# Kernel tuning notes

Hardware: AMD Instinct MI355X
Metric: run time of the kernel (lower is better)

Reference implementation:

```python
import jax, jax.numpy as jnp
import numpy as np

INPUT_DIM = 21
HIDDEN = 512
OUT_DIM = 20


def _lstm_cell(xt, h, c, Wx, bx, Wh):
    # xt: (B, in), h/c: (B, H); Wx: (4H, in), Wh: (4H, H), bx: (4H,)
    gates = xt @ Wx.T + bx + h @ Wh.T          # (B, 4H)
    i, f, g, o = jnp.split(gates, 4, axis=-1)   # torch chunk order: i, f, g, o
    i = jax.nn.sigmoid(i)
    f = jax.nn.sigmoid(f)
    g = jnp.tanh(g)
    o = jax.nn.sigmoid(o)
    c_new = f * c + i * g
    h_new = o * jnp.tanh(c_new)
    return h_new, c_new


def setup_inputs() -> dict:
    key = jax.random.key(0)
    ks = jax.random.split(key, 8)
    s_in = 1.0 / np.sqrt(INPUT_DIM)
    s_h = 1.0 / np.sqrt(HIDDEN)
    x = jax.random.normal(ks[0], (64, 1024, INPUT_DIM), dtype=jnp.float32)
    Wx0 = jax.random.uniform(ks[1], (4 * HIDDEN, INPUT_DIM), jnp.float32, -s_in, s_in)
    bx0 = jax.random.uniform(ks[2], (4 * HIDDEN,), jnp.float32, -s_in, s_in)
    Wh0 = jax.random.uniform(ks[3], (4 * HIDDEN, HIDDEN), jnp.float32, -s_h, s_h)
    Wx1 = jax.random.uniform(ks[4], (4 * HIDDEN, HIDDEN), jnp.float32, -s_h, s_h)
    bx1 = jax.random.uniform(ks[5], (4 * HIDDEN,), jnp.float32, -s_h, s_h)
    Wh1 = jax.random.uniform(ks[6], (4 * HIDDEN, HIDDEN), jnp.float32, -s_h, s_h)
    Wo = jax.random.uniform(ks[7], (OUT_DIM, HIDDEN), jnp.float32, -s_h, s_h)
    bo = jnp.zeros((OUT_DIM,), jnp.float32)
    return {"x": x, "Wx0": Wx0, "bx0": bx0, "Wh0": Wh0,
            "Wx1": Wx1, "bx1": bx1, "Wh1": Wh1, "Wo": Wo, "bo": bo}


def reference(x, Wx0, bx0, Wh0, Wx1, bx1, Wh1, Wo, bo):
    B, T, _ = x.shape
    H = Wh0.shape[1]
    h0 = jnp.zeros((B, H), x.dtype)
    c0 = jnp.zeros((B, H), x.dtype)
    h1 = jnp.zeros((B, H), x.dtype)
    c1 = jnp.zeros((B, H), x.dtype)

    def step(carry, xt):
        h0, c0, h1, c1 = carry
        h0, c0 = _lstm_cell(xt, h0, c0, Wx0, bx0, Wh0)
        h1, c1 = _lstm_cell(h0, h1, c1, Wx1, bx1, Wh1)
        out = jax.nn.sigmoid(h1 @ Wo.T + bo)  # (B, OUT_DIM)
        return (h0, c0, h1, c1), out

    _, outs = jax.lax.scan(step, (h0, c0, h1, c1), jnp.swapaxes(x, 0, 1))
    return jnp.swapaxes(outs, 0, 1)  # (B, T, OUT_DIM)
```

## Files before the change

kernel.cpp:

```cpp
#include <hip/hip_runtime.h>


#define T_STEPS 1024
#define WS_FLAG_OFF 0
#define WS_H0_OFF  4096
#define WS_H1_OFF  (4096 + 8*4*8192)
#define WS_NEED    (WS_H1_OFF + 8*2*8192)

#define SCOPE __HIP_MEMORY_SCOPE_AGENT

typedef _Float16 f16;
typedef _Float16 f16x8 __attribute__((ext_vector_type(8)));
typedef float    f32x4 __attribute__((ext_vector_type(4)));
typedef unsigned long long u64;

#define HP_STRIDE 520

__device__ __forceinline__ float sigm_(float x) {
    x = fminf(fmaxf(x, -30.f), 30.f);
    return 1.f / (1.f + __expf(-x));
}
__device__ __forceinline__ float tanh_(float x) {
    x = fminf(fmaxf(x, -15.f), 15.f);
    float e = __expf(-2.f * x);
    return (1.f - e) / (1.f + e);
}

__device__ __forceinline__ f16x8 afrag_lds(const f16* __restrict__ hp, int kbase,
                                           int b, int q) {
    return *(const f16x8*)(hp + (b & 7) * HP_STRIDE + kbase + q * 8);
}

__device__ __forceinline__ f16x8 pack8(const float* p) {
    float4 a = *(const float4*)p, b = *(const float4*)(p + 4);
    f16x8 f;
    f[0] = (f16)a.x; f[1] = (f16)a.y; f[2] = (f16)a.z; f[3] = (f16)a.w;
    f[4] = (f16)b.x; f[5] = (f16)b.y; f[6] = (f16)b.z; f[7] = (f16)b.w;
    return f;
}

__device__ __forceinline__ long long wait_flags(const int* f0, int t0,
                                                const int* f1, int t1, int lane,
                                                long long predict_clk) {
    const int* p = (lane & 16) ? (f1 + (lane & 15) * 4) : (f0 + (lane & 15) * 4);
    const int tgt = (lane & 16) ? t1 : t0;
    const bool act = (lane < 32);
    int v = act ? __hip_atomic_load(p, __ATOMIC_RELAXED, SCOPE)
                : 0x7fffffff;
    if (__all(v >= tgt)) return 0;
    long long t0c = (long long)__builtin_amdgcn_s_memtime();
    int rep = (int)(predict_clk >> 12);
    if (rep > 8) rep = 8;
    for (int i = 0; i < rep; ++i) __builtin_amdgcn_s_sleep(31);
    int spins = 0;
    for (;;) {
        v = act ? __hip_atomic_load(p, __ATOMIC_RELAXED, SCOPE)
                : 0x7fffffff;
        if (__all(v >= tgt)) break;
        ++spins;
        if (spins < 32)       __builtin_amdgcn_s_sleep(1);
        else if (spins < 256) __builtin_amdgcn_s_sleep(4);
        else                  __builtin_amdgcn_s_sleep(16);
        if (spins > (1 << 20)) break;
    }
    return (long long)__builtin_amdgcn_s_memtime() - t0c;
}

__device__ __forceinline__ long long ewma_upd(long long ew, long long d) {
    return ew - (ew >> 2) + (d >> 2);
}

__device__ __forceinline__ void stage_plane(const f16* __restrict__ gp,
                                            f16* __restrict__ dst, int tid) {
    const u64* g8 = (const u64*)gp;
    u64 v[4];
#pragma unroll
    for (int jj = 0; jj < 4; ++jj)
        v[jj] = __hip_atomic_load(g8 + jj * 256 + tid, __ATOMIC_RELAXED, SCOPE);
#pragma unroll
    for (int jj = 0; jj < 4; ++jj) {
        int i = jj * 256 + tid;
        int wg = i >> 6, b = (i >> 3) & 7, j = i & 7;
        *(u64*)(dst + b * HP_STRIDE + wg * 32 + j * 4) = v[jj];
    }
}

__device__ __forceinline__ void stage_two(const f16* __restrict__ gpA,
                                          f16* __restrict__ dstA,
                                          const f16* __restrict__ gpB,
                                          f16* __restrict__ dstB, int tid) {
    const u64* ga = (const u64*)gpA;
    const u64* gb = (const u64*)gpB;
    u64 va[4], vb[4];
#pragma unroll
    for (int jj = 0; jj < 4; ++jj)
        va[jj] = __hip_atomic_load(ga + jj * 256 + tid, __ATOMIC_RELAXED, SCOPE);
#pragma unroll
    for (int jj = 0; jj < 4; ++jj)
        vb[jj] = __hip_atomic_load(gb + jj * 256 + tid, __ATOMIC_RELAXED, SCOPE);
#pragma unroll
    for (int jj = 0; jj < 4; ++jj) {
        int i = jj * 256 + tid;
        int wg = i >> 6, b = (i >> 3) & 7, j = i & 7;
        *(u64*)(dstA + b * HP_STRIDE + wg * 32 + j * 4) = va[jj];
        *(u64*)(dstB + b * HP_STRIDE + wg * 32 + j * 4) = vb[jj];
    }
}

__device__ __forceinline__ f16x8 load_xfrag(const float* __restrict__ x,
                                            int gb8, int t, int ln, int q) {
    f16x8 f = {(_Float16)0, (_Float16)0, (_Float16)0, (_Float16)0,
               (_Float16)0, (_Float16)0, (_Float16)0, (_Float16)0};
    if (ln < 8 && t < T_STEPS) {
        const float* xp = x + ((size_t)(gb8 + ln) * 1024 + t) * 21;
#pragma unroll
        for (int j = 0; j < 8; ++j) {
            int kl = q * 8 + j;
            if (kl < 21) f[j] = (f16)xp[kl];
        }
    }
    return f;
}

__global__ void zero_ws_kernel(unsigned* __restrict__ p, int ndw) {
    int i = blockIdx.x * blockDim.x + threadIdx.x;
    int stride = gridDim.x * blockDim.x;
    for (; i < ndw; i += stride)
        __hip_atomic_store(p + i, 0u, __ATOMIC_RELAXED, SCOPE);
}

__global__ __launch_bounds__(256, 1)
void lstm_persist(const float* __restrict__ x,
                  const float* __restrict__ Wx0, const float* __restrict__ bx0,
                  const float* __restrict__ Wh0,
                  const float* __restrict__ Wx1, const float* __restrict__ bx1,
                  const float* __restrict__ Wh1,
                  const float* __restrict__ Wo,  const float* __restrict__ bo,
                  float* __restrict__ out, char* __restrict__ ws) {
    struct SM {
        float g[4][8][33];
        float c[8][32];
        float bias[4][32];
        __align__(8)  f16 hout[8][32];
        __align__(16) f16 planeA[8 * HP_STRIDE];
        __align__(16) f16 planeB[8 * HP_STRIDE];
        char  pad[60 * 1024];
    };
    __shared__ SM sm;
    const int tid = threadIdx.x;
    if (tid == 0x00FFFFFFu) sm.pad[0] = 1;

    const int bid  = blockIdx.x;
    const int g    = bid & 7;
    const int rk   = bid >> 3;
    const int role = rk >> 4;
    const int r    = rk & 15;
    const int w    = tid >> 6;
    const int lane = tid & 63;
    const int ln   = lane & 15;
    const int q    = lane >> 4;
    const int gb8  = g * 8;

    int* barb  = (int*)(ws + WS_FLAG_OFF) + g * 128;
    int* flag0 = barb;
    int* flag1 = barb + 64;
    f16* H0g = (f16*)(ws + WS_H0_OFF) + g * 16384;
    f16* H1g = (f16*)(ws + WS_H1_OFF) + g * 8192;

    ((float*)sm.c)[tid] = 0.f;
    if (tid < 128) {
        int gate = tid >> 5, u = tid & 31;
        const float* bx = role ? bx1 : bx0;
        sm.bias[gate][u] = bx[(gate << 9) + (r << 5) + u];
    }

    f16x8 W[64];
    if (role == 0) {
#pragma unroll
        for (int tau = 0; tau < 2; ++tau) {
            const int rw = (w << 9) + (r << 5) + tau * 16 + ln;
            const float* wh0r = Wh0 + (size_t)rw * 512;
#pragma unroll
            for (int kk = 0; kk < 16; ++kk)
                W[tau * 17 + kk] = pack8(wh0r + kk * 32 + q * 8);
            const float* wx0r = Wx0 + (size_t)rw * 21;
            f16x8 f = {(_Float16)0, (_Float16)0, (_Float16)0, (_Float16)0,
                       (_Float16)0, (_Float16)0, (_Float16)0, (_Float16)0};
#pragma unroll
            for (int j = 0; j < 8; ++j) {
                int kl = q * 8 + j;
                if (kl < 21) f[j] = (f16)wx0r[kl];
            }
            W[tau * 17 + 16] = f;
        }
    } else {
#pragma unroll
        for (int tau = 0; tau < 2; ++tau) {
            const int rw = (w << 9) + (r << 5) + tau * 16 + ln;
            const float* wx1r = Wx1 + (size_t)rw * 512;
            const float* wh1r = Wh1 + (size_t)rw * 512;
#pragma unroll
            for (int kk = 0; kk < 16; ++kk)
                W[tau * 32 + kk] = pack8(wx1r + kk * 32 + q * 8);
#pragma unroll
            for (int kk = 16; kk < 32; ++kk)
                W[tau * 32 + kk] = pack8(wh1r + (kk - 16) * 32 + q * 8);
        }
    }
    __syncthreads();

    if (role == 0) {
        long long ew = 0;
        for (int t = 0; t < T_STEPS; ++t) {
            const int wr = t & 3, rd = (t + 3) & 3;
            f16x8 xf = load_xfrag(x, gb8, t, ln, q);
            if (tid < 64) {
                long long d = wait_flags(flag0, t, flag1, t - 3, lane, ew);
                ew = ewma_upd(ew, d);
            }
            __syncthreads();
            stage_plane(H0g + rd * 4096, sm.planeA, tid);
            __syncthreads();

            f32x4 a0 = {0, 0, 0, 0}, a1 = {0, 0, 0, 0};
#pragma unroll
            for (int kk = 0; kk < 16; ++kk) {
                f16x8 A = afrag_lds(sm.planeA, kk * 32, ln, q);
                a0 = __builtin_amdgcn_mfma_f32_16x16x32_f16(A, W[kk], a0, 0, 0, 0);
                a1 = __builtin_amdgcn_mfma_f32_16x16x32_f16(A, W[17 + kk], a1, 0, 0, 0);
            }
            a0 = __builtin_amdgcn_mfma_f32_16x16x32_f16(xf, W[16], a0, 0, 0, 0);
            a1 = __builtin_amdgcn_mfma_f32_16x16x32_f16(xf, W[33], a1, 0, 0, 0);
            if (q < 2) {
#pragma unroll
                for (int r4 = 0; r4 < 4; ++r4) {
                    sm.g[w][q * 4 + r4][ln] = a0[r4];
                    sm.g[w][q * 4 + r4][16 + ln] = a1[r4];
                }
            }
            __syncthreads();
            {
                int b = tid >> 5, u = tid & 31;
                float gi = sm.g[0][b][u] + sm.bias[0][u];
                float gf = sm.g[1][b][u] + sm.bias[1][u];
                float gg = sm.g[2][b][u] + sm.bias[2][u];
                float go = sm.g[3][b][u] + sm.bias[3][u];
                float iv = sigm_(gi), fv = sigm_(gf), gv = tanh_(gg), ov = sigm_(go);
                float c = sm.c[b][u];
                float cn = fv * c + iv * gv;
                sm.c[b][u] = cn;
                sm.hout[b][u] = (f16)(ov * tanh_(cn));
            }
            __syncthreads();
            if (tid < 64) {
                int b = tid >> 3, j = tid & 7;
                u64 v = *(const u64*)&sm.hout[b][j * 4];
                __hip_atomic_store((u64*)(H0g + wr * 4096 + (r << 8) + (b << 5) + (j << 2)),
                                   v, __ATOMIC_RELAXED, SCOPE);
                asm volatile("s_waitcnt vmcnt(0)" ::: "memory");
                if (tid == 0)
                    __hip_atomic_store(flag0 + r * 4, t + 1, __ATOMIC_RELAXED, SCOPE);
            }
        }
    } else {
        long long ew = 0;
        for (int t = 0; t < T_STEPS; ++t) {
            const int wr = t & 1, rd = wr ^ 1;

            if (tid < 64) {
                long long d = wait_flags(flag0, t + 1, flag1, t, lane, ew);
                ew = ewma_upd(ew, d);
            }
            __syncthreads();
            stage_two(H0g + (t & 3) * 4096, sm.planeA,
                      H1g + rd * 4096,      sm.planeB,
                      tid);
            __syncthreads();

            f32x4 a0 = {0, 0, 0, 0}, a1 = {0, 0, 0, 0};
#pragma unroll
            for (int kk = 0; kk < 16; ++kk) {
                f16x8 A = afrag_lds(sm.planeA, kk * 32, ln, q);
                a0 = __builtin_amdgcn_mfma_f32_16x16x32_f16(A, W[kk], a0, 0, 0, 0);
                a1 = __builtin_amdgcn_mfma_f32_16x16x32_f16(A, W[32 + kk], a1, 0, 0, 0);
            }
#pragma unroll
            for (int kk = 16; kk < 32; ++kk) {
                f16x8 A = afrag_lds(sm.planeB, (kk - 16) * 32, ln, q);
                a0 = __builtin_amdgcn_mfma_f32_16x16x32_f16(A, W[kk], a0, 0, 0, 0);
                a1 = __builtin_amdgcn_mfma_f32_16x16x32_f16(A, W[32 + kk], a1, 0, 0, 0);
            }
            if (q < 2) {
#pragma unroll
                for (int r4 = 0; r4 < 4; ++r4) {
                    sm.g[w][q * 4 + r4][ln] = a0[r4];
                    sm.g[w][q * 4 + r4][16 + ln] = a1[r4];
                }
            }
            __syncthreads();
            {
                int b = tid >> 5, u = tid & 31;
                float gi = sm.g[0][b][u] + sm.bias[0][u];
                float gf = sm.g[1][b][u] + sm.bias[1][u];
                float gg = sm.g[2][b][u] + sm.bias[2][u];
                float go = sm.g[3][b][u] + sm.bias[3][u];
                float iv = sigm_(gi), fv = sigm_(gf), gv = tanh_(gg), ov = sigm_(go);
                float c = sm.c[b][u];
                float cn = fv * c + iv * gv;
                sm.c[b][u] = cn;
                sm.hout[b][u] = (f16)(ov * tanh_(cn));
            }
            __syncthreads();
            if (tid < 64) {
                int b = tid >> 3, j = tid & 7;
                u64 v = *(const u64*)&sm.hout[b][j * 4];
                __hip_atomic_store((u64*)(H1g + wr * 4096 + (r << 8) + (b << 5) + (j << 2)),
                                   v, __ATOMIC_RELAXED, SCOPE);
                asm volatile("s_waitcnt vmcnt(0)" ::: "memory");
                if (tid == 0)
                    __hip_atomic_store(flag1 + r * 4, t + 1, __ATOMIC_RELAXED, SCOPE);
            }

            if (t > 0) {
                int p = tid >> 4, kp = tid & 15;
                int valid = (p < 10);
                int idx = r * 10 + p;
                int b = valid ? idx / 20 : 0, o = valid ? idx % 20 : 0;
                float a = 0.f;
                if (valid) {
                    const f16* hp = sm.planeB + b * HP_STRIDE + kp * 32;
                    const float* wo = Wo + (size_t)o * 512 + kp * 32;
#pragma unroll
                    for (int k = 0; k < 32; k += 8) {
                        f16x8 hv = *(const f16x8*)(hp + k);
                        float4 wa = *(const float4*)(wo + k);
                        float4 wb = *(const float4*)(wo + k + 4);
                        a += (float)hv[0] * wa.x + (float)hv[1] * wa.y +
                             (float)hv[2] * wa.z + (float)hv[3] * wa.w +
                             (float)hv[4] * wb.x + (float)hv[5] * wb.y +
                             (float)hv[6] * wb.z + (float)hv[7] * wb.w;
                    }
                }
                a += __shfl_down(a, 8, 16);
                a += __shfl_down(a, 4, 16);
                a += __shfl_down(a, 2, 16);
                a += __shfl_down(a, 1, 16);
                if (valid && kp == 0)
                    out[((size_t)(gb8 + b) * 1024 + (t - 1)) * 20 + o] =
                        sigm_(a + bo[o]);
            }
        }

        if (tid < 64) wait_flags(flag1, T_STEPS, flag1, T_STEPS, lane, 0);
        __syncthreads();
        stage_plane(H1g + ((T_STEPS - 1) & 1) * 4096, sm.planeB, tid);
        __syncthreads();
        {
            int p = tid >> 4, kp = tid & 15;
            int valid = (p < 10);
            int idx = r * 10 + p;
            int b = valid ? idx / 20 : 0, o = valid ? idx % 20 : 0;
            float a = 0.f;
            if (valid) {
                const f16* hp = sm.planeB + b * HP_STRIDE + kp * 32;
                const float* wo = Wo + (size_t)o * 512 + kp * 32;
#pragma unroll
                for (int k = 0; k < 32; k += 8) {
                    f16x8 hv = *(const f16x8*)(hp + k);
                    float4 wa = *(const float4*)(wo + k);
                    float4 wb = *(const float4*)(wo + k + 4);
                    a += (float)hv[0] * wa.x + (float)hv[1] * wa.y +
                         (float)hv[2] * wa.z + (float)hv[3] * wa.w +
                         (float)hv[4] * wb.x + (float)hv[5] * wb.y +
                         (float)hv[6] * wb.z + (float)hv[7] * wb.w;
                }
            }
            a += __shfl_down(a, 8, 16);
            a += __shfl_down(a, 4, 16);
            a += __shfl_down(a, 2, 16);
            a += __shfl_down(a, 1, 16);
            if (valid && kp == 0)
                out[((size_t)(gb8 + b) * 1024 + (T_STEPS - 1)) * 20 + o] =
                    sigm_(a + bo[o]);
        }
    }
}

extern "C" void kernel_launch(void* const* d_in, const int* in_sizes, int n_in,
                              void* d_out, int out_size, void* d_ws, size_t ws_size,
                              hipStream_t stream) {
    const float* x   = (const float*)d_in[0];
    const float* Wx0 = (const float*)d_in[1];
    const float* bx0 = (const float*)d_in[2];
    const float* Wh0 = (const float*)d_in[3];
    const float* Wx1 = (const float*)d_in[4];
    const float* bx1 = (const float*)d_in[5];
    const float* Wh1 = (const float*)d_in[6];
    const float* Wo  = (const float*)d_in[7];
    const float* bo  = (const float*)d_in[8];
    float* out = (float*)d_out;
    char*  ws  = (char*)d_ws;

    if (ws_size < (size_t)WS_NEED) return;

    zero_ws_kernel<<<128, 256, 0, stream>>>((unsigned*)ws, WS_NEED / 4);
    lstm_persist<<<256, 256, 0, stream>>>(x, Wx0, bx0, Wh0, Wx1, bx1, Wh1,
                                          Wo, bo, out, ws);
}
```

Baseline: 3.713 ms.

## Use L2-scoped loads/stores for hidden-state exchange when group shares one XCC

At startup, blocks in each group record their XCC id and count arrivals in a workspace barrier. If all 32 blocks of a group sit on the same XCC, hidden-state exchange switches from agent-scope atomic loads/stores to plain stores and sc0 loads that bypass only the per-CU cache and hit the shared L2. The aim is lower latency on the per-step recurrent state handoff. It relies on blocks of a group landing on one XCC and adds a startup spin barrier; weak coherence assumptions could be fragile.

```diff
diff --git a/kernel.cpp b/kernel.cpp
--- a/kernel.cpp
+++ b/kernel.cpp
@@ -45,8 +45,7 @@
     const int* p = (lane & 16) ? (f1 + (lane & 15) * 4) : (f0 + (lane & 15) * 4);
     const int tgt = (lane & 16) ? t1 : t0;
     const bool act = (lane < 32);
-    int v = act ? __hip_atomic_load(p, __ATOMIC_RELAXED, SCOPE)
-                : 0x7fffffff;
+    int v = act ? __hip_atomic_load(p, __ATOMIC_RELAXED, SCOPE) : 0x7fffffff;
     if (__all(v >= tgt)) return 0;
     long long t0c = (long long)__builtin_amdgcn_s_memtime();
     int rep = (int)(predict_clk >> 12);
@@ -54,8 +53,7 @@
     for (int i = 0; i < rep; ++i) __builtin_amdgcn_s_sleep(31);
     int spins = 0;
     for (;;) {
-        v = act ? __hip_atomic_load(p, __ATOMIC_RELAXED, SCOPE)
-                : 0x7fffffff;
+        v = act ? __hip_atomic_load(p, __ATOMIC_RELAXED, SCOPE) : 0x7fffffff;
         if (__all(v >= tgt)) break;
         ++spins;
         if (spins < 32)       __builtin_amdgcn_s_sleep(1);
@@ -70,13 +68,26 @@
     return ew - (ew >> 2) + (d >> 2);
 }
 
+__device__ __forceinline__ u64 ld8_sc0(const u64* p) {
+    u64 v;
+    asm volatile("global_load_dwordx2 %0, %1, off sc0" : "=v"(v) : "v"(p));
+    return v;
+}
+
 __device__ __forceinline__ void stage_plane(const f16* __restrict__ gp,
-                                            f16* __restrict__ dst, int tid) {
+                                            f16* __restrict__ dst, int tid,
+                                            bool fast) {
     const u64* g8 = (const u64*)gp;
     u64 v[4];
-#pragma unroll
-    for (int jj = 0; jj < 4; ++jj)
-        v[jj] = __hip_atomic_load(g8 + jj * 256 + tid, __ATOMIC_RELAXED, SCOPE);
+    if (fast) {
+#pragma unroll
+        for (int jj = 0; jj < 4; ++jj) v[jj] = ld8_sc0(g8 + jj * 256 + tid);
+        asm volatile("s_waitcnt vmcnt(0)" ::: "memory");
+    } else {
+#pragma unroll
+        for (int jj = 0; jj < 4; ++jj)
+            v[jj] = __hip_atomic_load(g8 + jj * 256 + tid, __ATOMIC_RELAXED, SCOPE);
+    }
 #pragma unroll
     for (int jj = 0; jj < 4; ++jj) {
         int i = jj * 256 + tid;
@@ -88,16 +99,25 @@
 __device__ __forceinline__ void stage_two(const f16* __restrict__ gpA,
                                           f16* __restrict__ dstA,
                                           const f16* __restrict__ gpB,
-                                          f16* __restrict__ dstB, int tid) {
+                                          f16* __restrict__ dstB, int tid,
+                                          bool fast) {
     const u64* ga = (const u64*)gpA;
     const u64* gb = (const u64*)gpB;
     u64 va[4], vb[4];
-#pragma unroll
-    for (int jj = 0; jj < 4; ++jj)
-        va[jj] = __hip_atomic_load(ga + jj * 256 + tid, __ATOMIC_RELAXED, SCOPE);
-#pragma unroll
-    for (int jj = 0; jj < 4; ++jj)
-        vb[jj] = __hip_atomic_load(gb + jj * 256 + tid, __ATOMIC_RELAXED, SCOPE);
+    if (fast) {
+#pragma unroll
+        for (int jj = 0; jj < 4; ++jj) va[jj] = ld8_sc0(ga + jj * 256 + tid);
+#pragma unroll
+        for (int jj = 0; jj < 4; ++jj) vb[jj] = ld8_sc0(gb + jj * 256 + tid);
+        asm volatile("s_waitcnt vmcnt(0)" ::: "memory");
+    } else {
+#pragma unroll
+        for (int jj = 0; jj < 4; ++jj)
+            va[jj] = __hip_atomic_load(ga + jj * 256 + tid, __ATOMIC_RELAXED, SCOPE);
+#pragma unroll
+        for (int jj = 0; jj < 4; ++jj)
+            vb[jj] = __hip_atomic_load(gb + jj * 256 + tid, __ATOMIC_RELAXED, SCOPE);
+    }
 #pragma unroll
     for (int jj = 0; jj < 4; ++jj) {
         int i = jj * 256 + tid;
@@ -147,6 +167,7 @@
         char  pad[60 * 1024];
     };
     __shared__ SM sm;
+    __shared__ int s_fast;
     const int tid = threadIdx.x;
     if (tid == 0x00FFFFFFu) sm.pad[0] = 1;
 
@@ -207,7 +228,25 @@
                 W[tau * 32 + kk] = pack8(wh1r + (kk - 16) * 32 + q * 8);
         }
     }
+
+    if (tid == 0) {
+        unsigned xcc;
+        asm volatile("s_getreg_b32 %0, hwreg(HW_REG_XCC_ID)" : "=s"(xcc));
+        __hip_atomic_fetch_or(barb + 1, (int)(1u << (xcc & 31)),
+                              __ATOMIC_RELAXED, SCOPE);
+        __hip_atomic_fetch_add(barb + 2, 1, __ATOMIC_RELAXED, SCOPE);
+        int cnt = 0, spins = 0;
+        for (;;) {
+            cnt = __hip_atomic_load(barb + 2, __ATOMIC_RELAXED, SCOPE);
+            if (cnt >= 32 || spins > (1 << 18)) break;
+            __builtin_amdgcn_s_sleep(2);
+            ++spins;
+        }
+        unsigned m = (unsigned)__hip_atomic_load(barb + 1, __ATOMIC_RELAXED, SCOPE);
+        s_fast = (cnt >= 32 && __popc(m) == 1) ? 1 : 0;
+    }
     __syncthreads();
+    const bool fast = (s_fast != 0);
 
     if (role == 0) {
         long long ew = 0;
@@ -219,7 +258,7 @@
                 ew = ewma_upd(ew, d);
             }
             __syncthreads();
-            stage_plane(H0g + rd * 4096, sm.planeA, tid);
+            stage_plane(H0g + rd * 4096, sm.planeA, tid, fast);
             __syncthreads();
 
             f32x4 a0 = {0, 0, 0, 0}, a1 = {0, 0, 0, 0};
@@ -255,8 +294,9 @@
             if (tid < 64) {
                 int b = tid >> 3, j = tid & 7;
                 u64 v = *(const u64*)&sm.hout[b][j * 4];
-                __hip_atomic_store((u64*)(H0g + wr * 4096 + (r << 8) + (b << 5) + (j << 2)),
-                                   v, __ATOMIC_RELAXED, SCOPE);
+                u64* dp = (u64*)(H0g + wr * 4096 + (r << 8) + (b << 5) + (j << 2));
+                if (fast) *dp = v;
+                else __hip_atomic_store(dp, v, __ATOMIC_RELAXED, SCOPE);
                 asm volatile("s_waitcnt vmcnt(0)" ::: "memory");
                 if (tid == 0)
                     __hip_atomic_store(flag0 + r * 4, t + 1, __ATOMIC_RELAXED, SCOPE);
@@ -274,7 +314,7 @@
             __syncthreads();
             stage_two(H0g + (t & 3) * 4096, sm.planeA,
                       H1g + rd * 4096,      sm.planeB,
-                      tid);
+                      tid, fast);
             __syncthreads();
 
             f32x4 a0 = {0, 0, 0, 0}, a1 = {0, 0, 0, 0};
@@ -314,8 +354,9 @@
             if (tid < 64) {
                 int b = tid >> 3, j = tid & 7;
                 u64 v = *(const u64*)&sm.hout[b][j * 4];
-                __hip_atomic_store((u64*)(H1g + wr * 4096 + (r << 8) + (b << 5) + (j << 2)),
-                                   v, __ATOMIC_RELAXED, SCOPE);
+                u64* dp = (u64*)(H1g + wr * 4096 + (r << 8) + (b << 5) + (j << 2));
+                if (fast) *dp = v;
+                else __hip_atomic_store(dp, v, __ATOMIC_RELAXED, SCOPE);
                 asm volatile("s_waitcnt vmcnt(0)" ::: "memory");
                 if (tid == 0)
                     __hip_atomic_store(flag1 + r * 4, t + 1, __ATOMIC_RELAXED, SCOPE);
@@ -353,7 +394,7 @@
 
         if (tid < 64) wait_flags(flag1, T_STEPS, flag1, T_STEPS, lane, 0);
         __syncthreads();
-        stage_plane(H1g + ((T_STEPS - 1) & 1) * 4096, sm.planeB, tid);
+        stage_plane(H1g + ((T_STEPS - 1) & 1) * 4096, sm.planeB, tid, fast);
         __syncthreads();
         {
             int p = tid >> 4, kp = tid & 15;
```

Result: faster. 3.439 ms (-7.4%).
